# Performance work log

Measured on AMD Instinct MI355X. Metric: run time of the kernel, lower is better.

The kernel has to match this reference:

```python
import jax, jax.numpy as jnp
import numpy as np

NUM_HEADS = 16
MASKED_BIAS = -10000.0


def setup_inputs() -> dict:
    key = jax.random.key(0)
    k1, k2, k3 = jax.random.split(key, 3)
    B, S, D = 2, 2048, 1024
    return {
        "hidden_states": jax.random.normal(k1, (B, S, D), dtype=jnp.float32),
        "c_attn_w": jax.random.normal(k2, (D, 3 * D), dtype=jnp.float32) * 0.02,
        "c_attn_b": jnp.zeros((3 * D,), dtype=jnp.float32),
        "c_proj_w": jax.random.normal(k3, (D, D), dtype=jnp.float32) * 0.02,
        "c_proj_b": jnp.zeros((D,), dtype=jnp.float32),
    }


def reference(hidden_states, c_attn_w, c_attn_b, c_proj_w, c_proj_b):
    B, S, D = hidden_states.shape
    H = NUM_HEADS
    hd = D // H

    qkv = hidden_states @ c_attn_w + c_attn_b  # [B, S, 3D]
    q, k, v = jnp.split(qkv, 3, axis=-1)

    def split_heads(t):
        return t.reshape(B, S, H, hd).transpose(0, 2, 1, 3)  # [B, H, S, hd]

    q, k, v = split_heads(q), split_heads(k), split_heads(v)

    attn_weights = jnp.einsum("bhqd,bhkd->bhqk", q, k)
    attn_weights = attn_weights / jnp.sqrt(jnp.float32(hd))
    # multiplicative causal mask, matching eager GPT2: w*mask + (-1e4)*(1-mask)
    causal = jnp.tril(jnp.ones((S, S), dtype=attn_weights.dtype))  # [S, S]
    attn_weights = attn_weights * causal + MASKED_BIAS * (1.0 - causal)
    attn_weights = jax.nn.softmax(attn_weights, axis=-1)

    attn_output = jnp.einsum("bhqk,bhkd->bhqd", attn_weights, v)
    attn_output = attn_output.transpose(0, 2, 1, 3).reshape(B, S, D)
    attn_output = attn_output @ c_proj_w + c_proj_b
    return attn_output, attn_weights
```

## Files before the change

kernel.cpp:

```cpp
#include <hip/hip_runtime.h>


typedef __bf16 bf16_t;
typedef bf16_t bf16x8 __attribute__((ext_vector_type(8)));
typedef float f32x4 __attribute__((ext_vector_type(4)));
typedef unsigned short ushort8 __attribute__((ext_vector_type(8)));
typedef unsigned short ushort4v __attribute__((ext_vector_type(4)));

#define SEQ 2048
#define DMODEL 1024
#define MTOT 4096

#define AS1 __attribute__((address_space(1)))
#define AS3 __attribute__((address_space(3)))

__device__ __forceinline__ unsigned short f2bf(float f) {
  return __builtin_bit_cast(unsigned short, (bf16_t)f);
}
__device__ __forceinline__ float bf2f(unsigned short u) {
  return __builtin_bit_cast(float, (unsigned)u << 16);
}
__device__ __forceinline__ bf16x8 ldb8(const unsigned short* p) {
  return __builtin_bit_cast(bf16x8, *(const ushort8*)p);
}
__device__ __forceinline__ f32x4 mfma16(bf16x8 a, bf16x8 b, f32x4 c) {
  return __builtin_amdgcn_mfma_f32_16x16x32_bf16(a, b, c, 0, 0, 0);
}
__device__ __forceinline__ void gload16(const unsigned short* g, unsigned short* l) {
  __builtin_amdgcn_global_load_lds((AS1 const void*)g, (AS3 void*)l, 16, 0, 0);
}

__global__ __launch_bounds__(256) void cast_kernel(const float* __restrict__ in,
                                                   unsigned short* __restrict__ out) {
  int i = blockIdx.x * 256 + threadIdx.x;
  float4 v = ((const float4*)in)[i];
  ushort4v o;
  o[0] = f2bf(v.x); o[1] = f2bf(v.y); o[2] = f2bf(v.z); o[3] = f2bf(v.w);
  ((ushort4v*)out)[i] = o;
}

__global__ __launch_bounds__(256) void transpose_cast_kernel(const float* __restrict__ in,
                                                             unsigned short* __restrict__ out,
                                                             int R, int C) {
  __shared__ float tile[32][33];
  int c0 = blockIdx.x * 32, r0 = blockIdx.y * 32;
  int tx = threadIdx.x & 31, ty = threadIdx.x >> 5;
#pragma unroll
  for (int i = 0; i < 4; ++i)
    tile[ty + i * 8][tx] = in[(size_t)(r0 + ty + i * 8) * C + c0 + tx];
  __syncthreads();
#pragma unroll
  for (int i = 0; i < 4; ++i)
    out[(size_t)(c0 + ty + i * 8) * R + r0 + tx] = f2bf(tile[tx][ty + i * 8]);
}

template <int EPI>
__global__ __launch_bounds__(256) void gemm128(
    const unsigned short* __restrict__ A, const unsigned short* __restrict__ BT,
    const float* __restrict__ bias, float* __restrict__ outF,
    unsigned short* __restrict__ qws, unsigned short* __restrict__ kws,
    unsigned short* __restrict__ vws, int M, int N, int K) {
  __shared__ unsigned short Alds[128 * 32];
  __shared__ unsigned short Blds[128 * 32];
  int m0 = blockIdx.x * 128, n0 = blockIdx.y * 128;
  int t = threadIdx.x;
  int l = t & 63, j = l & 15, g = l >> 4;
  int w = t >> 6, wr = w >> 1, wc = w & 1;

  f32x4 acc[4][4];
#pragma unroll
  for (int mi = 0; mi < 4; ++mi)
#pragma unroll
    for (int st = 0; st < 4; ++st)
#pragma unroll
      for (int r = 0; r < 4; ++r) acc[mi][st][r] = 0.f;

  int srow = t >> 2;
  int scol = (t & 3) * 8;
  const unsigned short* aB0 = A + (size_t)(m0 + srow) * K + scol;
  const unsigned short* aB1 = aB0 + (size_t)64 * K;
  const unsigned short* bB0 = BT + (size_t)(n0 + srow) * K + scol;
  const unsigned short* bB1 = bB0 + (size_t)64 * K;
  unsigned short* aL0 = &Alds[srow * 32 + scol];
  unsigned short* aL1 = aL0 + 64 * 32;
  unsigned short* bL0 = &Blds[srow * 32 + scol];
  unsigned short* bL1 = bL0 + 64 * 32;

  for (int k0 = 0; k0 < K; k0 += 32) {
    __syncthreads();
    gload16(aB0 + k0, aL0);
    gload16(aB1 + k0, aL1);
    gload16(bB0 + k0, bL0);
    gload16(bB1 + k0, bL1);
    __syncthreads();
    bf16x8 af[4], bfr[4];
#pragma unroll
    for (int mi = 0; mi < 4; ++mi) af[mi] = ldb8(&Alds[(wr * 64 + mi * 16 + j) * 32 + g * 8]);
#pragma unroll
    for (int st = 0; st < 4; ++st) bfr[st] = ldb8(&Blds[(wc * 64 + st * 16 + j) * 32 + g * 8]);
#pragma unroll
    for (int mi = 0; mi < 4; ++mi)
#pragma unroll
      for (int st = 0; st < 4; ++st) acc[mi][st] = mfma16(af[mi], bfr[st], acc[mi][st]);
  }

#pragma unroll
  for (int st = 0; st < 4; ++st) {
    int n = n0 + wc * 64 + st * 16 + j;
    float bv = bias[n];
#pragma unroll
    for (int mi = 0; mi < 4; ++mi)
#pragma unroll
      for (int r = 0; r < 4; ++r) {
        int m = m0 + wr * 64 + mi * 16 + g * 4 + r;
        float val = acc[mi][st][r] + bv;
        if (EPI == 1) {
          outF[(size_t)m * N + n] = val;
        } else {
          int region = n >> 10;
          int h = (n & 1023) >> 6;
          int d = n & 63;
          int bb = m >> 11, s = m & 2047;
          int bh = bb * 16 + h;
          if (region == 0) qws[(((size_t)bh) * SEQ + s) * 64 + d] = f2bf(val * 0.125f);
          else if (region == 1) kws[(((size_t)bh) * SEQ + s) * 64 + d] = f2bf(val);
          else vws[(((size_t)bh) * 64 + d) * SEQ + s] = f2bf(val);
        }
      }
  }
}

__global__ __launch_bounds__(256) void attn_kernel(
    const unsigned short* __restrict__ qg, const unsigned short* __restrict__ kg,
    const unsigned short* __restrict__ vg, float* __restrict__ outw,
    unsigned short* __restrict__ ointer) {
  __shared__ unsigned short Klds[64][72];
  __shared__ unsigned short Vlds[64][72];
  __shared__ unsigned short Plds[4][16][72];

  int qt = (gridDim.x - 1) - blockIdx.x;
  int bh = blockIdx.y;
  int b = bh >> 4, h = bh & 15;
  int t = threadIdx.x;
  int w = t >> 6, l = t & 63, j = l & 15, g = l >> 4;

  const unsigned short* qb = qg + (size_t)bh * SEQ * 64;
  const unsigned short* kb = kg + (size_t)bh * SEQ * 64;
  const unsigned short* vb = vg + (size_t)bh * SEQ * 64;
  float* outrow = outw + (size_t)bh * SEQ * SEQ;

  int qr_a = qt * 64 + w * 16 + j;
  bf16x8 qa0 = ldb8(&qb[(size_t)qr_a * 64 + g * 8]);
  bf16x8 qa1 = ldb8(&qb[(size_t)qr_a * 64 + 32 + g * 8]);

  int qrow0 = qt * 64 + w * 16 + g * 4;

  float lpart[4] = {0.f, 0.f, 0.f, 0.f};

  int skey = t >> 2;
  int sc = (t & 3) * 8;

  for (int kt = 0; kt <= qt; ++kt) {
    __syncthreads();
    {
      const unsigned short* src = &kb[(size_t)(kt * 64 + skey) * 64];
      *(ushort8*)&Klds[skey][sc] = *(const ushort8*)&src[sc];
      *(ushort8*)&Klds[skey][sc + 32] = *(const ushort8*)&src[sc + 32];
    }
    __syncthreads();
    f32x4 sacc[4];
#pragma unroll
    for (int st = 0; st < 4; ++st)
#pragma unroll
      for (int r = 0; r < 4; ++r) sacc[st][r] = 0.f;
#pragma unroll
    for (int st = 0; st < 4; ++st) {
      bf16x8 kf0 = ldb8(&Klds[st * 16 + j][g * 8]);
      bf16x8 kf1 = ldb8(&Klds[st * 16 + j][32 + g * 8]);
      sacc[st] = mfma16(qa0, kf0, sacc[st]);
      sacc[st] = mfma16(qa1, kf1, sacc[st]);
    }
    bool diag = (kt == qt);
#pragma unroll
    for (int r = 0; r < 4; ++r) {
      int qrow = qrow0 + r;
#pragma unroll
      for (int st = 0; st < 4; ++st) {
        float p = __expf(sacc[st][r]);
        if (diag) {
          int kc = kt * 64 + st * 16 + j;
          p = (kc > qrow) ? 0.f : p;
        }
        lpart[r] += p;
      }
    }
  }

  float linv[4];
#pragma unroll
  for (int r = 0; r < 4; ++r) {
    float sum = lpart[r];
#pragma unroll
    for (int o = 1; o < 16; o <<= 1) sum += __shfl_xor(sum, o);
    linv[r] = 1.f / sum;
  }

  f32x4 oacc[4];
#pragma unroll
  for (int st = 0; st < 4; ++st)
#pragma unroll
    for (int r = 0; r < 4; ++r) oacc[st][r] = 0.f;

  int prow = l >> 2;
  int pch = l & 3;

  for (int kt = 0; kt < SEQ / 64; ++kt) {
    if (kt <= qt) {
      __syncthreads();
      {
        const unsigned short* src = &kb[(size_t)(kt * 64 + skey) * 64];
        *(ushort8*)&Klds[skey][sc] = *(const ushort8*)&src[sc];
        *(ushort8*)&Klds[skey][sc + 32] = *(const ushort8*)&src[sc + 32];
        const unsigned short* vsrc = &vb[(size_t)skey * SEQ + kt * 64];
        *(ushort8*)&Vlds[skey][sc] = *(const ushort8*)&vsrc[sc];
        *(ushort8*)&Vlds[skey][sc + 32] = *(const ushort8*)&vsrc[sc + 32];
      }
      __syncthreads();
      f32x4 sacc[4];
#pragma unroll
      for (int st = 0; st < 4; ++st)
#pragma unroll
        for (int r = 0; r < 4; ++r) sacc[st][r] = 0.f;
#pragma unroll
      for (int st = 0; st < 4; ++st) {
        bf16x8 kf0 = ldb8(&Klds[st * 16 + j][g * 8]);
        bf16x8 kf1 = ldb8(&Klds[st * 16 + j][32 + g * 8]);
        sacc[st] = mfma16(qa0, kf0, sacc[st]);
        sacc[st] = mfma16(qa1, kf1, sacc[st]);
      }
      bool diag = (kt == qt);
#pragma unroll
      for (int st = 0; st < 4; ++st) {
#pragma unroll
        for (int r = 0; r < 4; ++r) {
          int qrow = qrow0 + r;
          int kc = kt * 64 + st * 16 + j;
          float p = __expf(sacc[st][r]) * linv[r];
          if (diag) p = (kc > qrow) ? 0.f : p;
          Plds[w][g * 4 + r][st * 16 + j] = f2bf(p);
        }
      }
#pragma unroll
      for (int it = 0; it < 2; ++it) {
        int ch = pch + it * 4;
        ushort8 pv = *(const ushort8*)&Plds[w][prow][ch * 8];
        float4 f0, f1;
        f0.x = bf2f(pv[0]); f0.y = bf2f(pv[1]); f0.z = bf2f(pv[2]); f0.w = bf2f(pv[3]);
        f1.x = bf2f(pv[4]); f1.y = bf2f(pv[5]); f1.z = bf2f(pv[6]); f1.w = bf2f(pv[7]);
        float* dst = &outrow[(size_t)(qt * 64 + w * 16 + prow) * SEQ + kt * 64 + ch * 8];
        ((float4*)dst)[0] = f0;
        ((float4*)dst)[1] = f1;
      }
      bf16x8 pa0 = ldb8(&Plds[w][j][g * 8]);
      bf16x8 pa1 = ldb8(&Plds[w][j][32 + g * 8]);
#pragma unroll
      for (int st = 0; st < 4; ++st) {
        bf16x8 vf0 = ldb8(&Vlds[st * 16 + j][g * 8]);
        bf16x8 vf1 = ldb8(&Vlds[st * 16 + j][32 + g * 8]);
        oacc[st] = mfma16(pa0, vf0, oacc[st]);
        oacc[st] = mfma16(pa1, vf1, oacc[st]);
      }
    } else {
      int row = qt * 64 + w * 16 + (l >> 2);
      int c0 = kt * 64 + (l & 3) * 16;
      float4 z = make_float4(0.f, 0.f, 0.f, 0.f);
      float4* zp = (float4*)&outrow[(size_t)row * SEQ + c0];
      zp[0] = z; zp[1] = z; zp[2] = z; zp[3] = z;
    }
  }

#pragma unroll
  for (int st = 0; st < 4; ++st)
#pragma unroll
    for (int r = 0; r < 4; ++r) {
      int qrow = qrow0 + r;
      int d = st * 16 + j;
      ointer[((size_t)b * SEQ + qrow) * DMODEL + h * 64 + d] = f2bf(oacc[st][r]);
    }
}

extern "C" void kernel_launch(void* const* d_in, const int* in_sizes, int n_in,
                              void* d_out, int out_size, void* d_ws, size_t ws_size,
                              hipStream_t stream) {
  const float* hidden = (const float*)d_in[0];
  const float* w_attn = (const float*)d_in[1];
  const float* b_attn = (const float*)d_in[2];
  const float* w_proj = (const float*)d_in[3];
  const float* b_proj = (const float*)d_in[4];

  float* out_attn = (float*)d_out;
  float* out_w = out_attn + (size_t)MTOT * DMODEL;

  char* ws = (char*)d_ws;
  unsigned short* hbf = (unsigned short*)(ws);
  unsigned short* w1T = (unsigned short*)(ws + 8388608);
  unsigned short* w2T = (unsigned short*)(ws + 14680064);
  unsigned short* qws = (unsigned short*)(ws + 16777216);
  unsigned short* kws = (unsigned short*)(ws + 25165824);
  unsigned short* vws = (unsigned short*)(ws + 33554432);

  cast_kernel<<<4096, 256, 0, stream>>>(hidden, hbf);
  transpose_cast_kernel<<<dim3(96, 32), 256, 0, stream>>>(w_attn, w1T, 1024, 3072);
  transpose_cast_kernel<<<dim3(32, 32), 256, 0, stream>>>(w_proj, w2T, 1024, 1024);
  gemm128<0><<<dim3(32, 24), 256, 0, stream>>>(hbf, w1T, b_attn, nullptr, qws, kws, vws,
                                               MTOT, 3 * DMODEL, DMODEL);
  attn_kernel<<<dim3(32, 32), 256, 0, stream>>>(qws, kws, vws, out_w, hbf);
  gemm128<1><<<dim3(32, 8), 256, 0, stream>>>(hbf, w2T, b_proj, out_attn, nullptr, nullptr,
                                              nullptr, MTOT, DMODEL, DMODEL);
}
```

Measured before the change: 273.2 us.

## Split attention into single-pass flash kernel and separate weight-writing kernel

The attention kernel now computes the row sums and unnormalized P·V together in one pass over keys, normalizing the output at the end, and stores the inverse row sums to workspace. A new grid-parallel kernel recomputes QK^T per 128x128 tile and writes the normalized attention weights, or zeros for tiles above the diagonal. This removes the second sequential pass and moves the large weight-matrix write out of the imbalanced causal loop into a balanced grid. The cost is one extra launch, a recomputation of QK^T, and reuse of the w1T workspace region for the row sums.

```diff
diff --git a/kernel.cpp b/kernel.cpp
--- a/kernel.cpp
+++ b/kernel.cpp
@@ -16,9 +16,6 @@
 
 __device__ __forceinline__ unsigned short f2bf(float f) {
   return __builtin_bit_cast(unsigned short, (bf16_t)f);
-}
-__device__ __forceinline__ float bf2f(unsigned short u) {
-  return __builtin_bit_cast(float, (unsigned)u << 16);
 }
 __device__ __forceinline__ bf16x8 ldb8(const unsigned short* p) {
   return __builtin_bit_cast(bf16x8, *(const ushort8*)p);
@@ -130,15 +127,15 @@
   }
 }
 
-__global__ __launch_bounds__(256) void attn_kernel(
+__global__ __launch_bounds__(256) void attn_flash(
     const unsigned short* __restrict__ qg, const unsigned short* __restrict__ kg,
-    const unsigned short* __restrict__ vg, float* __restrict__ outw,
+    const unsigned short* __restrict__ vg, float* __restrict__ linvb,
     unsigned short* __restrict__ ointer) {
   __shared__ unsigned short Klds[64][72];
   __shared__ unsigned short Vlds[64][72];
-  __shared__ unsigned short Plds[4][16][72];
-
-  int qt = (gridDim.x - 1) - blockIdx.x;
+  __shared__ unsigned short Plds[4][16 * 72];
+
+  int qt = 31 - blockIdx.x;
   int bh = blockIdx.y;
   int b = bh >> 4, h = bh & 15;
   int t = threadIdx.x;
@@ -147,7 +144,6 @@
   const unsigned short* qb = qg + (size_t)bh * SEQ * 64;
   const unsigned short* kb = kg + (size_t)bh * SEQ * 64;
   const unsigned short* vb = vg + (size_t)bh * SEQ * 64;
-  float* outrow = outw + (size_t)bh * SEQ * SEQ;
 
   int qr_a = qt * 64 + w * 16 + j;
   bf16x8 qa0 = ldb8(&qb[(size_t)qr_a * 64 + g * 8]);
@@ -155,10 +151,15 @@
 
   int qrow0 = qt * 64 + w * 16 + g * 4;
 
-  float lpart[4] = {0.f, 0.f, 0.f, 0.f};
-
   int skey = t >> 2;
   int sc = (t & 3) * 8;
+
+  float lpart[4] = {0.f, 0.f, 0.f, 0.f};
+  f32x4 oacc[4];
+#pragma unroll
+  for (int st = 0; st < 4; ++st)
+#pragma unroll
+    for (int r = 0; r < 4; ++r) oacc[st][r] = 0.f;
 
   for (int kt = 0; kt <= qt; ++kt) {
     __syncthreads();
@@ -166,6 +167,9 @@
       const unsigned short* src = &kb[(size_t)(kt * 64 + skey) * 64];
       *(ushort8*)&Klds[skey][sc] = *(const ushort8*)&src[sc];
       *(ushort8*)&Klds[skey][sc + 32] = *(const ushort8*)&src[sc + 32];
+      const unsigned short* vsrc = &vb[(size_t)skey * SEQ + kt * 64];
+      *(ushort8*)&Vlds[skey][sc] = *(const ushort8*)&vsrc[sc];
+      *(ushort8*)&Vlds[skey][sc + 32] = *(const ushort8*)&vsrc[sc + 32];
     }
     __syncthreads();
     f32x4 sacc[4];
@@ -182,17 +186,25 @@
     }
     bool diag = (kt == qt);
 #pragma unroll
-    for (int r = 0; r < 4; ++r) {
-      int qrow = qrow0 + r;
-#pragma unroll
-      for (int st = 0; st < 4; ++st) {
+    for (int st = 0; st < 4; ++st)
+#pragma unroll
+      for (int r = 0; r < 4; ++r) {
         float p = __expf(sacc[st][r]);
         if (diag) {
           int kc = kt * 64 + st * 16 + j;
-          p = (kc > qrow) ? 0.f : p;
+          p = (kc > qrow0 + r) ? 0.f : p;
         }
         lpart[r] += p;
+        Plds[w][(g * 4 + r) * 72 + st * 16 + j] = f2bf(p);
       }
+    bf16x8 pa0 = ldb8(&Plds[w][j * 72 + g * 8]);
+    bf16x8 pa1 = ldb8(&Plds[w][j * 72 + 32 + g * 8]);
+#pragma unroll
+    for (int st = 0; st < 4; ++st) {
+      bf16x8 vf0 = ldb8(&Vlds[st * 16 + j][g * 8]);
+      bf16x8 vf1 = ldb8(&Vlds[st * 16 + j][32 + g * 8]);
+      oacc[st] = mfma16(pa0, vf0, oacc[st]);
+      oacc[st] = mfma16(pa1, vf1, oacc[st]);
     }
   }
 
@@ -204,88 +216,90 @@
     for (int o = 1; o < 16; o <<= 1) sum += __shfl_xor(sum, o);
     linv[r] = 1.f / sum;
   }
-
-  f32x4 oacc[4];
-#pragma unroll
-  for (int st = 0; st < 4; ++st)
-#pragma unroll
-    for (int r = 0; r < 4; ++r) oacc[st][r] = 0.f;
-
-  int prow = l >> 2;
-  int pch = l & 3;
-
-  for (int kt = 0; kt < SEQ / 64; ++kt) {
-    if (kt <= qt) {
-      __syncthreads();
-      {
-        const unsigned short* src = &kb[(size_t)(kt * 64 + skey) * 64];
-        *(ushort8*)&Klds[skey][sc] = *(const ushort8*)&src[sc];
-        *(ushort8*)&Klds[skey][sc + 32] = *(const ushort8*)&src[sc + 32];
-        const unsigned short* vsrc = &vb[(size_t)skey * SEQ + kt * 64];
-        *(ushort8*)&Vlds[skey][sc] = *(const ushort8*)&vsrc[sc];
-        *(ushort8*)&Vlds[skey][sc + 32] = *(const ushort8*)&vsrc[sc + 32];
-      }
-      __syncthreads();
-      f32x4 sacc[4];
-#pragma unroll
-      for (int st = 0; st < 4; ++st)
-#pragma unroll
-        for (int r = 0; r < 4; ++r) sacc[st][r] = 0.f;
-#pragma unroll
-      for (int st = 0; st < 4; ++st) {
-        bf16x8 kf0 = ldb8(&Klds[st * 16 + j][g * 8]);
-        bf16x8 kf1 = ldb8(&Klds[st * 16 + j][32 + g * 8]);
-        sacc[st] = mfma16(qa0, kf0, sacc[st]);
-        sacc[st] = mfma16(qa1, kf1, sacc[st]);
-      }
-      bool diag = (kt == qt);
-#pragma unroll
-      for (int st = 0; st < 4; ++st) {
-#pragma unroll
-        for (int r = 0; r < 4; ++r) {
-          int qrow = qrow0 + r;
-          int kc = kt * 64 + st * 16 + j;
-          float p = __expf(sacc[st][r]) * linv[r];
-          if (diag) p = (kc > qrow) ? 0.f : p;
-          Plds[w][g * 4 + r][st * 16 + j] = f2bf(p);
-        }
-      }
-#pragma unroll
-      for (int it = 0; it < 2; ++it) {
-        int ch = pch + it * 4;
-        ushort8 pv = *(const ushort8*)&Plds[w][prow][ch * 8];
-        float4 f0, f1;
-        f0.x = bf2f(pv[0]); f0.y = bf2f(pv[1]); f0.z = bf2f(pv[2]); f0.w = bf2f(pv[3]);
-        f1.x = bf2f(pv[4]); f1.y = bf2f(pv[5]); f1.z = bf2f(pv[6]); f1.w = bf2f(pv[7]);
-        float* dst = &outrow[(size_t)(qt * 64 + w * 16 + prow) * SEQ + kt * 64 + ch * 8];
-        ((float4*)dst)[0] = f0;
-        ((float4*)dst)[1] = f1;
-      }
-      bf16x8 pa0 = ldb8(&Plds[w][j][g * 8]);
-      bf16x8 pa1 = ldb8(&Plds[w][j][32 + g * 8]);
-#pragma unroll
-      for (int st = 0; st < 4; ++st) {
-        bf16x8 vf0 = ldb8(&Vlds[st * 16 + j][g * 8]);
-        bf16x8 vf1 = ldb8(&Vlds[st * 16 + j][32 + g * 8]);
-        oacc[st] = mfma16(pa0, vf0, oacc[st]);
-        oacc[st] = mfma16(pa1, vf1, oacc[st]);
-      }
-    } else {
-      int row = qt * 64 + w * 16 + (l >> 2);
-      int c0 = kt * 64 + (l & 3) * 16;
-      float4 z = make_float4(0.f, 0.f, 0.f, 0.f);
-      float4* zp = (float4*)&outrow[(size_t)row * SEQ + c0];
-      zp[0] = z; zp[1] = z; zp[2] = z; zp[3] = z;
-    }
-  }
-
+  if (j == 0) {
+#pragma unroll
+    for (int r = 0; r < 4; ++r) linvb[(size_t)bh * SEQ + qrow0 + r] = linv[r];
+  }
 #pragma unroll
   for (int st = 0; st < 4; ++st)
 #pragma unroll
     for (int r = 0; r < 4; ++r) {
       int qrow = qrow0 + r;
       int d = st * 16 + j;
-      ointer[((size_t)b * SEQ + qrow) * DMODEL + h * 64 + d] = f2bf(oacc[st][r]);
+      ointer[((size_t)b * SEQ + qrow) * DMODEL + h * 64 + d] = f2bf(oacc[st][r] * linv[r]);
+    }
+}
+
+__global__ __launch_bounds__(256) void pwrite_kernel(
+    const unsigned short* __restrict__ qg, const unsigned short* __restrict__ kg,
+    const float* __restrict__ linvb, float* __restrict__ outw) {
+  int kj = blockIdx.x, qi = blockIdx.y, bh = blockIdx.z;
+  float* outrow = outw + (size_t)bh * SEQ * SEQ;
+  int t = threadIdx.x;
+
+  if (kj > qi) {
+    int row = qi * 128 + (t >> 1);
+    float4* dst = (float4*)&outrow[(size_t)row * SEQ + kj * 128 + (t & 1) * 64];
+    float4 z = make_float4(0.f, 0.f, 0.f, 0.f);
+#pragma unroll
+    for (int i = 0; i < 16; ++i) dst[i] = z;
+    return;
+  }
+
+  __shared__ unsigned short Qlds[128 * 72];
+  __shared__ unsigned short Klds[128 * 72];
+  int l = t & 63, j = l & 15, g = l >> 4;
+  int w = t >> 6, wr = w >> 1, wc = w & 1;
+
+  {
+    int srow = t >> 1;
+    int cb = (t & 1) * 32;
+    const unsigned short* qsrc = qg + ((size_t)bh * SEQ + qi * 128 + srow) * 64 + cb;
+    const unsigned short* ksrc = kg + ((size_t)bh * SEQ + kj * 128 + srow) * 64 + cb;
+#pragma unroll
+    for (int i = 0; i < 4; ++i) {
+      *(ushort8*)&Qlds[srow * 72 + cb + i * 8] = *(const ushort8*)&qsrc[i * 8];
+      *(ushort8*)&Klds[srow * 72 + cb + i * 8] = *(const ushort8*)&ksrc[i * 8];
+    }
+  }
+  __syncthreads();
+
+  f32x4 acc[4][4];
+#pragma unroll
+  for (int mi = 0; mi < 4; ++mi)
+#pragma unroll
+    for (int st = 0; st < 4; ++st)
+#pragma unroll
+      for (int r = 0; r < 4; ++r) acc[mi][st][r] = 0.f;
+
+#pragma unroll
+  for (int kk = 0; kk < 2; ++kk) {
+    bf16x8 af[4], bfr[4];
+#pragma unroll
+    for (int mi = 0; mi < 4; ++mi)
+      af[mi] = ldb8(&Qlds[(wr * 64 + mi * 16 + j) * 72 + kk * 32 + g * 8]);
+#pragma unroll
+    for (int st = 0; st < 4; ++st)
+      bfr[st] = ldb8(&Klds[(wc * 64 + st * 16 + j) * 72 + kk * 32 + g * 8]);
+#pragma unroll
+    for (int mi = 0; mi < 4; ++mi)
+#pragma unroll
+      for (int st = 0; st < 4; ++st) acc[mi][st] = mfma16(af[mi], bfr[st], acc[mi][st]);
+  }
+
+#pragma unroll
+  for (int mi = 0; mi < 4; ++mi)
+#pragma unroll
+    for (int r = 0; r < 4; ++r) {
+      int qrow = qi * 128 + wr * 64 + mi * 16 + g * 4 + r;
+      float lv = linvb[(size_t)bh * SEQ + qrow];
+      float* orow = &outrow[(size_t)qrow * SEQ];
+#pragma unroll
+      for (int st = 0; st < 4; ++st) {
+        int kc = kj * 128 + wc * 64 + st * 16 + j;
+        float p = (kc > qrow) ? 0.f : __expf(acc[mi][st][r]) * lv;
+        orow[kc] = p;
+      }
     }
 }
 
@@ -308,13 +322,15 @@
   unsigned short* qws = (unsigned short*)(ws + 16777216);
   unsigned short* kws = (unsigned short*)(ws + 25165824);
   unsigned short* vws = (unsigned short*)(ws + 33554432);
+  float* linvb = (float*)(ws + 8388608);
 
   cast_kernel<<<4096, 256, 0, stream>>>(hidden, hbf);
   transpose_cast_kernel<<<dim3(96, 32), 256, 0, stream>>>(w_attn, w1T, 1024, 3072);
   transpose_cast_kernel<<<dim3(32, 32), 256, 0, stream>>>(w_proj, w2T, 1024, 1024);
   gemm128<0><<<dim3(32, 24), 256, 0, stream>>>(hbf, w1T, b_attn, nullptr, qws, kws, vws,
                                                MTOT, 3 * DMODEL, DMODEL);
-  attn_kernel<<<dim3(32, 32), 256, 0, stream>>>(qws, kws, vws, out_w, hbf);
+  attn_flash<<<dim3(32, 32), 256, 0, stream>>>(qws, kws, vws, linvb, hbf);
+  pwrite_kernel<<<dim3(16, 16, 32), 256, 0, stream>>>(qws, kws, linvb, out_w);
   gemm128<1><<<dim3(32, 8), 256, 0, stream>>>(hbf, w2T, b_proj, out_attn, nullptr, nullptr,
                                               nullptr, MTOT, DMODEL, DMODEL);
 }
```

Measured after the change: 304.3 us. 1.11x slower.
